# Kernel optimization log

Hardware: AMD Instinct MI355X
Metric: run time of the kernel (lower is better)

Reference implementation:

```python
import jax, jax.numpy as jnp
import numpy as np

G = 160          # dense lattice extent
N = 250000       # occupied voxels


def _offsets(vals):
    a, b, c = np.meshgrid(vals, vals, vals, indexing='ij')
    return np.stack([a.ravel(), b.ravel(), c.ravel()], axis=1)


def _build_kmap(src_lin_sorted, dst_coords, offsets, grid):
    # For each dst coord and kernel offset, find index of src coord (or -1).
    Nd, K = dst_coords.shape[0], offsets.shape[0]
    idx = np.full((Nd, K), -1, dtype=np.int64)
    for k in range(K):
        nb = dst_coords + offsets[k]
        valid = np.all((nb >= 0) & (nb < grid), axis=1)
        keys = (nb[valid, 0] * grid + nb[valid, 1]) * grid + nb[valid, 2]
        pos = np.searchsorted(src_lin_sorted, keys)
        pos_c = np.minimum(pos, len(src_lin_sorted) - 1)
        found = src_lin_sorted[pos_c] == keys
        vi = np.nonzero(valid)[0]
        idx[vi[found], k] = pos_c[found]
    return idx


def setup_inputs() -> dict:
    rng = np.random.default_rng(0)
    lin = np.sort(rng.choice(G ** 3, size=N, replace=False))
    coords = np.stack(np.unravel_index(lin, (G, G, G)), axis=1).astype(np.int64)
    off27 = _offsets(np.array([-1, 0, 1]))
    idx1 = _build_kmap(lin, coords, off27, G)          # k3/s1 on input lattice
    G2 = G // 2
    c2 = coords // 2
    lin2 = np.unique((c2[:, 0] * G2 + c2[:, 1]) * G2 + c2[:, 2])
    coords2 = np.stack(np.unravel_index(lin2, (G2, G2, G2)), axis=1).astype(np.int64)
    off8 = _offsets(np.array([0, 1]))
    idx_down = _build_kmap(lin, coords2 * 2, off8, G)  # k2/s2 downsample map
    idx2 = _build_kmap(lin2, coords2, off27, G2)       # k3/s1 on downsampled lattice

    key = jax.random.key(0)
    ks = jax.random.split(key, 12)

    def w(k, shape, fan_in):
        return jax.random.normal(k, shape, jnp.float32) * (1.0 / np.sqrt(fan_in))

    return {
        'x_feat': jax.random.normal(ks[0], (N, 64), jnp.float32),
        'f1_ref': jax.random.normal(ks[1], (N, 64), jnp.float32),
        'w1': w(ks[2], (27, 64, 64), 27 * 64), 'b1': jnp.zeros((64,), jnp.float32),
        'wd': w(ks[3], (8, 64, 32), 8 * 64), 'bd': jnp.zeros((32,), jnp.float32),
        'rw00': w(ks[4], (3, 27, 32, 8), 27 * 32), 'rb00': jnp.zeros((3, 8), jnp.float32),
        'rw01': w(ks[5], (3, 27, 8, 16), 27 * 8), 'rb01': jnp.zeros((3, 16), jnp.float32),
        'rw10': w(ks[6], (3, 32, 8), 32), 'rb10': jnp.zeros((3, 8), jnp.float32),
        'rw11': w(ks[7], (3, 27, 8, 8), 27 * 8), 'rb11': jnp.zeros((3, 8), jnp.float32),
        'rw12': w(ks[8], (3, 8, 16), 8), 'rb12': jnp.zeros((3, 16), jnp.float32),
        'w4': w(ks[9], (27, 32, 8), 27 * 32), 'b4': jnp.zeros((8,), jnp.float32),
        'idx1': jnp.asarray(idx1), 'idx_down': jnp.asarray(idx_down), 'idx2': jnp.asarray(idx2),
    }


def sparse_conv(feat, idx, W, b):
    # Minkowski sparse conv as gather-GEMM-accumulate over kernel offsets.
    # feat [Nin,Cin], idx [Nout,K] with -1 = no neighbor, W [K,Cin,Cout], b [Cout]
    def step(acc, xs):
        ik, Wk = xs  # [Nout], [Cin,Cout]
        g = jnp.where((ik >= 0)[:, None], feat[jnp.maximum(ik, 0)], 0.0)
        return acc + g @ Wk, None
    acc0 = jnp.zeros((idx.shape[0], W.shape[-1]), feat.dtype)
    out, _ = jax.lax.scan(step, acc0, (idx.T, W))
    return out + b


def reference(x_feat, f1_ref, w1, b1, wd, bd, rw00, rb00, rw01, rb01, rw10, rb10, rw11, rb11, rw12, rb12, w4, b4, idx1, idx_down, idx2):
    relu = jax.nn.relu
    x = x_feat + f1_ref                                  # f1_ref residual add
    out = relu(sparse_conv(x, idx1, w1, b1))             # conv1 + relu
    out = relu(sparse_conv(out, idx_down, wd, bd))       # down (k2/s2) + relu
    for i in range(3):                                   # InceptionResNet x block_layers
        out0 = sparse_conv(relu(sparse_conv(out, idx2, rw00[i], rb00[i])), idx2, rw01[i], rb01[i])
        t = relu(out @ rw10[i] + rb10[i])                # kernel-size-1 conv == linear
        t = relu(sparse_conv(t, idx2, rw11[i], rb11[i]))
        out1 = t @ rw12[i] + rb12[i]
        out = jnp.concatenate([out0, out1], axis=-1) + out
    return sparse_conv(out, idx2, w4, b4)                # enc4
```

## Files before the change

kernel.cpp:

```cpp
#include <hip/hip_runtime.h>
#include <cstdint>

typedef unsigned short u16;
typedef unsigned int   u32;

typedef __bf16 bf16_t;
typedef bf16_t bf16x8 __attribute__((ext_vector_type(8)));
typedef float  f32x16 __attribute__((ext_vector_type(16)));

__device__ __forceinline__ float bf2f(u16 v){ u32 u=((u32)v)<<16; float f; __builtin_memcpy(&f,&u,4); return f; }
__device__ __forceinline__ u16 f2bf(float f){ u32 u; __builtin_memcpy(&u,&f,4); u=(u+0x7FFFu+((u>>16)&1u))>>16; return (u16)u; }

__device__ __forceinline__ u16 cvt(const void* s, long long i, int fbf){
  return fbf ? ((const u16*)s)[i] : f2bf(((const float*)s)[i]);
}

__device__ __forceinline__ int xcd_swz(int bo, int nwg){
  const int q = nwg >> 3, r = nwg & 7;
  const int xcd = bo & 7, lin = bo >> 3;
  return (xcd < r ? xcd * (q + 1) : r * (q + 1) + (xcd - r) * q) + lin;
}

__global__ void detect_k(const u32* __restrict__ xf, const u32* __restrict__ ix,
                         int* __restrict__ flags){
  __shared__ int c0, c1;
  const int t = threadIdx.x;
  if (t == 0) { c0 = 0; c1 = 0; }
  __syncthreads();
  int a = 0, b = 0;
  for (int i = t; i < 1024; i += 256) {
    u32 w = xf[i];
    int e = (int)((w >> 7) & 0xFFu);
    if (e >= 100 && e <= 140) a++;
  }
  for (int i = t; i < 8192; i += 256) {
    u32 lo = ix[2 * i], hi = ix[2 * i + 1];
    if (lo != 0xFFFFFFFFu && hi != 0u && hi != 0xFFFFFFFFu) b++;
  }
  atomicAdd(&c0, a); atomicAdd(&c1, b);
  __syncthreads();
  if (t == 0) { flags[0] = (c0 >= 768) ? 1 : 0; flags[1] = (c1 == 0) ? 1 : 0; }
}

__global__ __launch_bounds__(256) void itr_k(
    const void* __restrict__ idx, int nK, int nKpad, int Nout, int nsrc,
    int Npad, int* __restrict__ dst, const int* __restrict__ flags){
  __shared__ int tile[28][257];
  const int f64 = flags[1];
  const int t = threadIdx.x;
  const int p0 = blockIdx.x * 256;
  const int32_t*  __restrict__ i32 = (const int32_t*)idx;
  const long long* __restrict__ i64 = (const long long*)idx;
  int pl = t / nK;
  int k  = t - pl * nK;
  const int dp = 256 / nK, dk = 256 - dp * nK;
  while (pl < 256) {
    const int p = p0 + pl;
    int j = -1;
    if (p < Nout) {
      const size_t ii = (size_t)p * nK + k;
      j = f64 ? (int)i64[ii] : i32[ii];
    }
    tile[k][pl] = (j < 0 || j > nsrc) ? nsrc : j;
    pl += dp; k += dk;
    if (k >= nK) { k -= nK; pl += 1; }
  }
  __syncthreads();
  for (int kk = 0; kk < nKpad; ++kk) {
    const int v = (kk < nK) ? tile[kk][t] : nsrc;
    dst[(size_t)kk * Npad + p0 + t] = v;
  }
}

template<int CIN, int NF, int NKP, int BCH>
__global__ __launch_bounds__(256) void gconv(
    const u16* __restrict__ src, int nsrc,
    const void* __restrict__ idx, int nK,
    const int* __restrict__ idxT, int Npad,
    const u16* __restrict__ BTf, int iters,
    const u16* __restrict__ bias,
    const u16* __restrict__ bias2, int b2off,
    const u16* __restrict__ resid,
    void* __restrict__ out, int ostride, int coloff, int Cout,
    int relu,
    u16* __restrict__ out2, int o2st, int o2off,
    int Nout, const int* __restrict__ flags, int out_ext)
{
  constexpr int SH = (CIN == 64) ? 7 : (CIN == 32) ? 6 : (CIN == 16) ? 5 : 4;
  constexpr int NB = (BCH == 0) ? 2 * NF : 1;
  __shared__ int idxL[NKP][256];
  __shared__ __align__(16) u16 BsL[(BCH > 0) ? BCH * NF * 512 : 8];

  const int tid = threadIdx.x;
  const int w = tid >> 6, l = tid & 63;
  const int lm = l & 31, lh = l >> 5;
  const int kloc = lh * 8;
  const int M0 = xcd_swz(blockIdx.x, gridDim.x) * 256;
  const int fbf = flags[0], f64 = flags[1];
  const int pl0 = 2 * w * 32 + lm;

  if (idxT) {
    for (int i = tid; i < NKP * 64; i += 256) {
      const int k = i >> 6, g = (i & 63) << 2;
      const uint4 v = *(const uint4*)(idxT + (size_t)k * Npad + M0 + g);
      *(int4*)&idxL[k][g] = make_int4((int)v.x << SH, (int)v.y << SH,
                                      (int)v.z << SH, (int)v.w << SH);
    }
  } else {
    for (int i = tid; i < NKP * 256; i += 256) {
      const int k = i >> 8, pl = i & 255, p = M0 + pl;
      int j = -1;
      if (k < nK && p < Nout) {
        const size_t ii = (size_t)p * nK + k;
        j = f64 ? (int)((const long long*)idx)[ii] : ((const int32_t*)idx)[ii];
      }
      const int r = (j < 0 || j > nsrc) ? nsrc : j;
      idxL[k][pl] = r << SH;
    }
  }
  if constexpr (BCH > 0) {
    for (int i = tid; i < BCH * NF * 64; i += 256)
      ((uint4*)BsL)[i] = ((const uint4*)BTf)[i];
  }
  __syncthreads();

  f32x16 acc[2][NF];
  #pragma unroll
  for (int mm = 0; mm < 2; ++mm)
    #pragma unroll
    for (int nf = 0; nf < NF; ++nf)
      #pragma unroll
      for (int e = 0; e < 16; ++e) acc[mm][nf][e] = 0.f;

  auto LD = [&](int it, uint4 (&A)[4], uint4 (&B)[NB]) {
    const int c0 = 2 * it;
    if constexpr (CIN >= 32) {
      const int k = (CIN == 64) ? (c0 >> 2) : (c0 >> 1);
      const int o0 = idxL[k][pl0];
      const int o1 = idxL[k][pl0 + 32];
      const char* s0 = (const char*)src + o0;
      const char* s1 = (const char*)src + o1;
      #pragma unroll
      for (int s = 0; s < 2; ++s) {
        const int c = c0 + s;
        const int ci2 = ((CIN == 64) ? (((c & 3) << 4) + kloc) : (((c & 1) << 4) + kloc)) * 2;
        A[s * 2 + 0] = *(const uint4*)(s0 + ci2);
        A[s * 2 + 1] = *(const uint4*)(s1 + ci2);
      }
    } else if constexpr (CIN == 16) {
      #pragma unroll
      for (int s = 0; s < 2; ++s) {
        const int k = c0 + s;
        const int o0 = idxL[k][pl0];
        const int o1 = idxL[k][pl0 + 32];
        A[s * 2 + 0] = *(const uint4*)((const char*)src + o0 + lh * 16);
        A[s * 2 + 1] = *(const uint4*)((const char*)src + o1 + lh * 16);
      }
    } else {
      #pragma unroll
      for (int s = 0; s < 2; ++s) {
        const int c = c0 + s;
        const int k = c * 2 + lh;
        const int o0 = idxL[k][pl0];
        const int o1 = idxL[k][pl0 + 32];
        A[s * 2 + 0] = *(const uint4*)((const char*)src + o0);
        A[s * 2 + 1] = *(const uint4*)((const char*)src + o1);
      }
    }
    if constexpr (BCH == 0) {
      #pragma unroll
      for (int s = 0; s < 2; ++s)
        #pragma unroll
        for (int nf = 0; nf < NF; ++nf)
          B[s * NF + nf] = *(const uint4*)(BTf + (((size_t)(c0 + s) * NF + nf) * 64 + l) * 8);
    }
  };

  auto MM = [&](int it, const uint4 (&A)[4], const uint4 (&B)[NB]) {
    const int c0 = 2 * it;
    #pragma unroll
    for (int s = 0; s < 2; ++s) {
      const bf16x8 a0 = __builtin_bit_cast(bf16x8, A[s * 2 + 0]);
      const bf16x8 a1 = __builtin_bit_cast(bf16x8, A[s * 2 + 1]);
      #pragma unroll
      for (int nf = 0; nf < NF; ++nf) {
        bf16x8 b;
        if constexpr (BCH > 0) b = *(const bf16x8*)&BsL[(((c0 + s) * NF + nf) * 64 + l) * 8];
        else                   b = __builtin_bit_cast(bf16x8, B[s * NF + nf]);
        acc[0][nf] = __builtin_amdgcn_mfma_f32_32x32x16_bf16(a0, b, acc[0][nf], 0, 0, 0);
        acc[1][nf] = __builtin_amdgcn_mfma_f32_32x32x16_bf16(a1, b, acc[1][nf], 0, 0, 0);
      }
    }
  };

  uint4 A0[4], A1[4], A2[4], B0[NB], B1[NB], B2[NB];
  LD(0, A0, B0);
  if (iters > 1) LD(1, A1, B1);
  for (int it = 0; it < iters; it += 3) {
    if (it + 2 < iters) LD(it + 2, A2, B2);
    MM(it, A0, B0);
    if (it + 3 < iters) LD(it + 3, A0, B0);
    if (it + 1 < iters) MM(it + 1, A1, B1);
    if (it + 4 < iters) LD(it + 4, A1, B1);
    if (it + 2 < iters) MM(it + 2, A2, B2);
  }

  const int fp32out = out_ext && !fbf;
  #pragma unroll
  for (int mm = 0; mm < 2; ++mm) {
    #pragma unroll
    for (int nf = 0; nf < NF; ++nf) {
      const int co = nf * 32 + lm;
      if (co >= Cout) continue;
      const float bv = (bias2 && co >= b2off) ? bf2f(bias2[co - b2off]) : bf2f(bias[co]);
      #pragma unroll
      for (int r = 0; r < 16; ++r) {
        const int m = (r & 3) + 8 * (r >> 2) + 4 * lh;
        const int p = M0 + (2 * w + mm) * 32 + m;
        if (p >= Nout) continue;
        float v = acc[mm][nf][r] + bv;
        if (out2 && co >= o2off) {
          if (v < 0.f) v = 0.f;
          out2[(size_t)p * o2st + (co - o2off)] = f2bf(v);
        } else {
          if (resid) v += bf2f(resid[(size_t)p * ostride + coloff + co]);
          if (relu && v < 0.f) v = 0.f;
          const size_t ofs = (size_t)p * ostride + coloff + co;
          if (fp32out) ((float*)out)[ofs] = v;
          else         ((u16*)out)[ofs] = f2bf(v);
        }
      }
    }
  }
}

struct PrepJob {
  const void* src; const void* src2; long long eoff, eoff2; u16* dst;
  int nK, Cin, Cout, COPAD, KKpad, mode, count;
};
struct PrepArgs { PrepJob j[19]; };

__global__ void prep_k(PrepArgs a, const int* __restrict__ flags){
  PrepJob jb = a.j[blockIdx.y];
  const int fbf = flags[0];
  if (jb.mode == 1) {
    for (int t = blockIdx.x * 256 + threadIdx.x; t < jb.count; t += gridDim.x * 256)
      jb.dst[t] = cvt(jb.src, jb.eoff + t, fbf);
    return;
  }
  const int total = jb.COPAD * jb.KKpad;
  const int kkmax = jb.nK * jb.Cin;
  if (jb.mode == 3) {
    for (int t = blockIdx.x * 256 + threadIdx.x; t < total; t += gridDim.x * 256) {
      const int e  = t & 7;
      const int lj = (t >> 3) & 63;
      const int chunk = t >> 9;
      const int co = lj & 31;
      const int kk = chunk * 16 + ((lj >> 5) << 3) + e;
      const int k = kk >> 4, ci = kk & 15;
      u16 v = 0;
      if (kk < kkmax && co < jb.Cout) {
        if (ci < 8 && co < 16)
          v = cvt(jb.src,  jb.eoff  + (long long)(k * 8 + ci) * 16 + co, fbf);
        else if (ci >= 8 && co >= 16)
          v = cvt(jb.src2, jb.eoff2 + (long long)(k * 8 + (ci - 8)) * 8 + (co - 16), fbf);
      }
      jb.dst[t] = v;
    }
    return;
  }
  const int NFj = jb.COPAD >> 5;
  for (int t = blockIdx.x * 256 + threadIdx.x; t < total; t += gridDim.x * 256) {
    const int e  = t & 7;
    const int lj = (t >> 3) & 63;
    const int cn = t >> 9;
    const int nf = cn & (NFj - 1);
    const int chunk = cn >> (NFj - 1);
    const int co = nf * 32 + (lj & 31);
    const int kk = chunk * 16 + ((lj >> 5) << 3) + e;
    u16 v = 0;
    if (co < jb.Cout && kk < kkmax)
      v = cvt(jb.src, jb.eoff + (long long)kk * jb.Cout + co, fbf);
    jb.dst[t] = v;
  }
}

__global__ void xsum_k(const void* __restrict__ xa, const void* __restrict__ xb,
                       u16* __restrict__ dst, int n8valid, int n8tot,
                       const int* __restrict__ flags){
  int t = blockIdx.x * 256 + threadIdx.x;
  if (t >= n8tot) return;
  const int fbf = flags[0];
  union { uint4 v; u16 h[8]; } O;
  if (t < n8valid) {
    if (fbf) {
      union { uint4 v; u16 h[8]; } A, B;
      A.v = ((const uint4*)xa)[t];
      B.v = ((const uint4*)xb)[t];
      #pragma unroll
      for (int e = 0; e < 8; ++e) O.h[e] = f2bf(bf2f(A.h[e]) + bf2f(B.h[e]));
    } else {
      const float4* fa = (const float4*)xa;
      const float4* fb = (const float4*)xb;
      float4 a0 = fa[2 * t], a1 = fa[2 * t + 1];
      float4 b0 = fb[2 * t], b1 = fb[2 * t + 1];
      O.h[0] = f2bf(a0.x + b0.x); O.h[1] = f2bf(a0.y + b0.y);
      O.h[2] = f2bf(a0.z + b0.z); O.h[3] = f2bf(a0.w + b0.w);
      O.h[4] = f2bf(a1.x + b1.x); O.h[5] = f2bf(a1.y + b1.y);
      O.h[6] = f2bf(a1.z + b1.z); O.h[7] = f2bf(a1.w + b1.w);
    }
  } else {
    O.v = make_uint4(0, 0, 0, 0);
  }
  ((uint4*)dst)[t] = O.v;
}

__global__ void zrows_k(u16* out1, int N, u16* od0, u16* od1, u16* ht, int N2){
  int t = threadIdx.x;
  if (t < 64) out1[(size_t)N * 64 + t] = 0;
  if (t < 32) od0[(size_t)N2 * 32 + t] = 0;
  if (t < 32) od1[(size_t)N2 * 32 + t] = 0;
  if (t < 16) ht[(size_t)N2 * 16 + t] = 0;
}

__global__ void t8lin_k(const u16* __restrict__ od, const u16* __restrict__ wsrc,
                        const u16* __restrict__ bsrc, u16* __restrict__ ht, int N2){
  __shared__ u16 wl[256];
  int t = threadIdx.x;
  wl[t] = wsrc[t];
  __syncthreads();
  int p = blockIdx.x * 256 + t;
  if (p >= N2) return;
  union { uint4 v[4]; u16 h[32]; } R;
  const uint4* rp = (const uint4*)(od + (size_t)p * 32);
  R.v[0] = rp[0]; R.v[1] = rp[1]; R.v[2] = rp[2]; R.v[3] = rp[3];
  float acc[8];
  #pragma unroll
  for (int o = 0; o < 8; ++o) acc[o] = bf2f(bsrc[o]);
  #pragma unroll
  for (int c = 0; c < 32; ++c) {
    float f = bf2f(R.h[c]);
    #pragma unroll
    for (int o = 0; o < 8; ++o) acc[o] += f * bf2f(wl[c * 8 + o]);
  }
  union { uint4 v; u16 h[8]; } O;
  #pragma unroll
  for (int o = 0; o < 8; ++o) { float v = acc[o]; if (v < 0.f) v = 0.f; O.h[o] = f2bf(v); }
  *(uint4*)(ht + (size_t)p * 16 + 8) = O.v;
}

__global__ void o1lin_k(const u16* __restrict__ t2, const u16* __restrict__ wsrc,
                        const u16* __restrict__ bsrc, const u16* __restrict__ odin,
                        u16* __restrict__ odout, int N2){
  __shared__ u16 wl[128];
  int t = threadIdx.x;
  if (t < 128) wl[t] = wsrc[t];
  __syncthreads();
  int p = blockIdx.x * 256 + t;
  if (p >= N2) return;
  union { uint4 v; u16 h[8]; } R; R.v = ((const uint4*)(t2 + (size_t)p * 8))[0];
  union { uint4 v[2]; u16 h[16]; } Rs;
  const uint4* rp = (const uint4*)(odin + (size_t)p * 32 + 16);
  Rs.v[0] = rp[0]; Rs.v[1] = rp[1];
  float acc[16];
  #pragma unroll
  for (int o = 0; o < 16; ++o) acc[o] = bf2f(bsrc[o]) + bf2f(Rs.h[o]);
  #pragma unroll
  for (int c = 0; c < 8; ++c) {
    float f = bf2f(R.h[c]);
    #pragma unroll
    for (int o = 0; o < 16; ++o) acc[o] += f * bf2f(wl[c * 16 + o]);
  }
  union { uint4 v[2]; u16 h[16]; } O;
  #pragma unroll
  for (int o = 0; o < 16; ++o) O.h[o] = f2bf(acc[o]);
  uint4* op = (uint4*)(odout + (size_t)p * 32 + 16);
  op[0] = O.v[0]; op[1] = O.v[1];
}

extern "C" void kernel_launch(void* const* d_in, const int* in_sizes, int n_in,
                              void* d_out, int out_size, void* d_ws, size_t ws_size,
                              hipStream_t stream) {
  const void* x_feat = d_in[0];
  const void* f1_ref = d_in[1];
  const void* w1   = d_in[2];
  const void* b1   = d_in[3];
  const void* wd   = d_in[4];
  const void* bd   = d_in[5];
  const void* rw00 = d_in[6];
  const void* rb00 = d_in[7];
  const void* rw01 = d_in[8];
  const void* rb01 = d_in[9];
  const void* rw10 = d_in[10];
  const void* rb10 = d_in[11];
  const void* rw11 = d_in[12];
  const void* rb11 = d_in[13];
  const void* rw12 = d_in[14];
  const void* rb12 = d_in[15];
  const void* w4   = d_in[16];
  const void* b4   = d_in[17];
  const void* idx1 = d_in[18];
  const void* idxd = d_in[19];
  const void* idx2 = d_in[20];

  const int N  = in_sizes[0] / 64;
  const int N2 = out_size / 8;

  const int nb1 = (N + 255) / 256;
  const int nb2 = (N2 + 255) / 256;
  const int Npad1 = nb1 * 256;
  const int Npad2 = nb2 * 256;

  size_t off = 0;
  auto carve = [&](size_t n) { void* p = (char*)d_ws + off; off = (off + n + 255) & ~(size_t)255; return p; };
  int* flags = (int*)carve(64 * sizeof(int));
  u16* xsum = (u16*)carve((size_t)(N + 1) * 64 * 2);
  u16* out1 = (u16*)carve((size_t)(N + 1) * 64 * 2);
  u16* od0  = (u16*)carve((size_t)(N2 + 1) * 32 * 2);
  u16* od1  = (u16*)carve((size_t)(N2 + 1) * 32 * 2);
  u16* ht   = (u16*)carve((size_t)(N2 + 1) * 16 * 2);
  u16* t2   = (u16*)carve((size_t)(N2 + 1) * 8 * 2);
  u16* smallw = (u16*)carve((size_t)2048 * 2);
  u16* BT1  = (u16*)carve((size_t)64 * 1728 * 2);
  u16* BTd  = (u16*)carve((size_t)32 * 512 * 2);
  u16* BT00 = (u16*)carve((size_t)3 * 32 * 864 * 2);
  u16* BTf1 = (u16*)carve((size_t)3 * 32 * 448 * 2);
  u16* BT4  = (u16*)carve((size_t)32 * 864 * 2);
  const size_t base_off = off;
  int* idx1T = (int*)carve((size_t)27 * Npad1 * 4);
  int* idxdT = (int*)carve((size_t)8  * Npad2 * 4);
  int* idx2T = (int*)carve((size_t)28 * Npad2 * 4);
  const int useT = (off <= ws_size);
  if (base_off > ws_size) return;
  if (!useT) { idx1T = nullptr; idxdT = nullptr; idx2T = nullptr; }

  u16* cb1   = smallw + 0;
  u16* cbd   = smallw + 64;
  u16* crb00 = smallw + 96;
  u16* crb01 = smallw + 120;
  u16* crb10 = smallw + 168;
  u16* crb11 = smallw + 192;
  u16* crb12 = smallw + 216;
  u16* cb4   = smallw + 264;
  u16* crw10 = smallw + 272;
  u16* crw12 = smallw + 1040;

  detect_k<<<1, 256, 0, stream>>>((const u32*)x_feat, (const u32*)idx1, flags);

  PrepArgs pa;
  pa.j[0]  = { w1, nullptr, 0, 0, BT1, 27, 64, 64, 64, 1728, 0, 0 };
  pa.j[1]  = { wd, nullptr, 0, 0, BTd,  8, 64, 32, 32,  512, 0, 0 };
  for (int i = 0; i < 3; ++i) {
    pa.j[2 + i] = { rw00, nullptr, (long long)i * 6912, 0,
                    BT00 + (size_t)i * 32 * 864, 27, 32, 8, 32, 864, 0, 0 };
    pa.j[5 + i] = { rw01, rw11, (long long)i * 3456, (long long)i * 1728,
                    BTf1 + (size_t)i * 32 * 448, 27, 16, 24, 32, 448, 3, 0 };
  }
  pa.j[8]  = { w4, nullptr, 0, 0, BT4, 27, 32, 8, 32, 864, 0, 0 };
  pa.j[9]  = { b1,   nullptr, 0, 0, cb1,   0,0,0,0,0, 1, 64 };
  pa.j[10] = { bd,   nullptr, 0, 0, cbd,   0,0,0,0,0, 1, 32 };
  pa.j[11] = { rb00, nullptr, 0, 0, crb00, 0,0,0,0,0, 1, 24 };
  pa.j[12] = { rb01, nullptr, 0, 0, crb01, 0,0,0,0,0, 1, 48 };
  pa.j[13] = { rb10, nullptr, 0, 0, crb10, 0,0,0,0,0, 1, 24 };
  pa.j[14] = { rb11, nullptr, 0, 0, crb11, 0,0,0,0,0, 1, 24 };
  pa.j[15] = { rb12, nullptr, 0, 0, crb12, 0,0,0,0,0, 1, 48 };
  pa.j[16] = { b4,   nullptr, 0, 0, cb4,   0,0,0,0,0, 1, 8 };
  pa.j[17] = { rw10, nullptr, 0, 0, crw10, 0,0,0,0,0, 1, 768 };
  pa.j[18] = { rw12, nullptr, 0, 0, crw12, 0,0,0,0,0, 1, 384 };
  prep_k<<<dim3(432, 19), 256, 0, stream>>>(pa, flags);

  if (useT) {
    itr_k<<<nb1, 256, 0, stream>>>(idx1, 27, 27, N,  N,  Npad1, idx1T, flags);
    itr_k<<<nb2, 256, 0, stream>>>(idxd,  8,  8, N2, N,  Npad2, idxdT, flags);
    itr_k<<<nb2, 256, 0, stream>>>(idx2, 27, 28, N2, N2, Npad2, idx2T, flags);
  }

  const int n8valid = N * 8, n8tot = (N + 1) * 8;
  xsum_k<<<(n8tot + 255) / 256, 256, 0, stream>>>(x_feat, f1_ref, xsum, n8valid, n8tot, flags);
  zrows_k<<<1, 256, 0, stream>>>(out1, N, od0, od1, ht, N2);

  gconv<64, 2, 27, 0><<<nb1, 256, 0, stream>>>(xsum, N, idx1, 27, idx1T, Npad1, BT1, 54,
                                               cb1, nullptr, 0, nullptr,
                                               out1, 64, 0, 64, 1, nullptr, 0, 0,
                                               N, flags, 0);
  gconv<64, 1, 8, 32><<<nb2, 256, 0, stream>>>(out1, N, idxd, 8, idxdT, Npad2, BTd, 16,
                                               cbd, nullptr, 0, nullptr,
                                               od0, 32, 0, 32, 1, nullptr, 0, 0,
                                               N2, flags, 0);
  for (int i = 0; i < 3; ++i) {
    u16* oin  = (i & 1) ? od1 : od0;
    u16* oout = (i & 1) ? od0 : od1;
    gconv<32, 1, 27, 0><<<nb2, 256, 0, stream>>>(oin, N2, idx2, 27, idx2T, Npad2,
                                                 BT00 + (size_t)i * 32 * 864, 27,
                                                 crb00 + i * 8, nullptr, 0, nullptr,
                                                 ht, 16, 0, 8, 1, nullptr, 0, 0,
                                                 N2, flags, 0);
    t8lin_k<<<nb2, 256, 0, stream>>>(oin, crw10 + i * 256, crb10 + i * 8, ht, N2);
    gconv<16, 1, 28, 0><<<nb2, 256, 0, stream>>>(ht, N2, idx2, 27, idx2T, Npad2,
                                                 BTf1 + (size_t)i * 32 * 448, 14,
                                                 crb01 + i * 16, crb11 + i * 8, 16, oin,
                                                 oout, 32, 0, 24, 0, t2, 8, 16,
                                                 N2, flags, 0);
    o1lin_k<<<nb2, 256, 0, stream>>>(t2, crw12 + i * 128, crb12 + i * 16, oin, oout, N2);
  }
  gconv<32, 1, 27, 0><<<nb2, 256, 0, stream>>>(od1, N2, idx2, 27, idx2T, Npad2, BT4, 27,
                                               cb4, nullptr, 0, nullptr,
                                               d_out, 8, 0, 8, 0, nullptr, 0, 0,
                                               N2, flags, 1);
}
```

Measured before the change: 698.5 us.

## Fuse 1x1 linear layers into sparse conv kernels and raise MFMA priority

The 1x1 linear rw10 is folded into the rw00 conv's weight matrix, placed at the center-tap rows as extra output columns, so one gconv produces both branches. The rw12 linear plus its residual is computed in an epilogue of the following conv through shared memory, which removes the t8lin_k and o1lin_k launches and the t2 intermediate buffer. It also raises wave priority around the MFMA blocks. The trade-off is extra shared memory, an extra barrier and wasted MMA columns for the fused linear.

```diff
diff --git a/kernel.cpp b/kernel.cpp
--- a/kernel.cpp
+++ b/kernel.cpp
@@ -72,7 +72,7 @@
   }
 }
 
-template<int CIN, int NF, int NKP, int BCH>
+template<int CIN, int NF, int NKP, int BCH, int L2>
 __global__ __launch_bounds__(256) void gconv(
     const u16* __restrict__ src, int nsrc,
     const void* __restrict__ idx, int nK,
@@ -84,12 +84,15 @@
     void* __restrict__ out, int ostride, int coloff, int Cout,
     int relu,
     u16* __restrict__ out2, int o2st, int o2off,
+    const u16* __restrict__ l2w, const u16* __restrict__ l2b,
     int Nout, const int* __restrict__ flags, int out_ext)
 {
   constexpr int SH = (CIN == 64) ? 7 : (CIN == 32) ? 6 : (CIN == 16) ? 5 : 4;
   constexpr int NB = (BCH == 0) ? 2 * NF : 1;
   __shared__ int idxL[NKP][256];
   __shared__ __align__(16) u16 BsL[(BCH > 0) ? BCH * NF * 512 : 8];
+  __shared__ u16 t2L[L2 ? 256 : 1][8];
+  __shared__ u16 l2wl[L2 ? 144 : 1];
 
   const int tid = threadIdx.x;
   const int w = tid >> 6, l = tid & 63;
@@ -121,6 +124,9 @@
   if constexpr (BCH > 0) {
     for (int i = tid; i < BCH * NF * 64; i += 256)
       ((uint4*)BsL)[i] = ((const uint4*)BTf)[i];
+  }
+  if constexpr (L2) {
+    if (tid < 144) l2wl[tid] = (tid < 128) ? l2w[tid] : l2b[tid - 128];
   }
   __syncthreads();
 
@@ -178,6 +184,7 @@
 
   auto MM = [&](int it, const uint4 (&A)[4], const uint4 (&B)[NB]) {
     const int c0 = 2 * it;
+    __builtin_amdgcn_s_setprio(1);
     #pragma unroll
     for (int s = 0; s < 2; ++s) {
       const bf16x8 a0 = __builtin_bit_cast(bf16x8, A[s * 2 + 0]);
@@ -191,6 +198,7 @@
         acc[1][nf] = __builtin_amdgcn_mfma_f32_32x32x16_bf16(a1, b, acc[1][nf], 0, 0, 0);
       }
     }
+    __builtin_amdgcn_s_setprio(0);
   };
 
   uint4 A0[4], A1[4], A2[4], B0[NB], B1[NB], B2[NB];
@@ -216,12 +224,14 @@
       #pragma unroll
       for (int r = 0; r < 16; ++r) {
         const int m = (r & 3) + 8 * (r >> 2) + 4 * lh;
-        const int p = M0 + (2 * w + mm) * 32 + m;
+        const int pl = (2 * w + mm) * 32 + m;
+        const int p = M0 + pl;
         if (p >= Nout) continue;
         float v = acc[mm][nf][r] + bv;
-        if (out2 && co >= o2off) {
+        if ((L2 || out2) && co >= o2off) {
           if (v < 0.f) v = 0.f;
-          out2[(size_t)p * o2st + (co - o2off)] = f2bf(v);
+          if constexpr (L2) t2L[pl][co - o2off] = f2bf(v);
+          else              out2[(size_t)p * o2st + (co - o2off)] = f2bf(v);
         } else {
           if (resid) v += bf2f(resid[(size_t)p * ostride + coloff + co]);
           if (relu && v < 0.f) v = 0.f;
@@ -232,13 +242,37 @@
       }
     }
   }
+
+  if constexpr (L2) {
+    __syncthreads();
+    const int p = M0 + tid;
+    if (p < Nout) {
+      union { uint4 v[2]; u16 h[16]; } Rs;
+      const uint4* rp = (const uint4*)(resid + (size_t)p * 32 + 16);
+      Rs.v[0] = rp[0]; Rs.v[1] = rp[1];
+      float a[16];
+      #pragma unroll
+      for (int o = 0; o < 16; ++o) a[o] = bf2f(l2wl[128 + o]) + bf2f(Rs.h[o]);
+      #pragma unroll
+      for (int c = 0; c < 8; ++c) {
+        const float f = bf2f(t2L[tid][c]);
+        #pragma unroll
+        for (int o = 0; o < 16; ++o) a[o] += f * bf2f(l2wl[c * 16 + o]);
+      }
+      union { uint4 v[2]; u16 h[16]; } O;
+      #pragma unroll
+      for (int o = 0; o < 16; ++o) O.h[o] = f2bf(a[o]);
+      uint4* op = (uint4*)((u16*)out + (size_t)p * 32 + 16);
+      op[0] = O.v[0]; op[1] = O.v[1];
+    }
+  }
 }
 
 struct PrepJob {
   const void* src; const void* src2; long long eoff, eoff2; u16* dst;
   int nK, Cin, Cout, COPAD, KKpad, mode, count;
 };
-struct PrepArgs { PrepJob j[19]; };
+struct PrepArgs { PrepJob j[18]; };
 
 __global__ void prep_k(PrepArgs a, const int* __restrict__ flags){
   PrepJob jb = a.j[blockIdx.y];
@@ -269,6 +303,25 @@
     }
     return;
   }
+  if (jb.mode == 4) {
+    for (int t = blockIdx.x * 256 + threadIdx.x; t < total; t += gridDim.x * 256) {
+      const int e  = t & 7;
+      const int lj = (t >> 3) & 63;
+      const int chunk = t >> 9;
+      const int co = lj & 31;
+      const int kk = chunk * 16 + ((lj >> 5) << 3) + e;
+      const int k = kk >> 5, ci = kk & 31;
+      u16 v = 0;
+      if (kk < kkmax) {
+        if (co < 8)
+          v = cvt(jb.src, jb.eoff + (long long)(k * 32 + ci) * 8 + co, fbf);
+        else if (co < 16 && k == 13)
+          v = cvt(jb.src2, jb.eoff2 + (long long)ci * 8 + (co - 8), fbf);
+      }
+      jb.dst[t] = v;
+    }
+    return;
+  }
   const int NFj = jb.COPAD >> 5;
   for (int t = blockIdx.x * 256 + threadIdx.x; t < total; t += gridDim.x * 256) {
     const int e  = t & 7;
@@ -321,61 +374,6 @@
   if (t < 32) od0[(size_t)N2 * 32 + t] = 0;
   if (t < 32) od1[(size_t)N2 * 32 + t] = 0;
   if (t < 16) ht[(size_t)N2 * 16 + t] = 0;
-}
-
-__global__ void t8lin_k(const u16* __restrict__ od, const u16* __restrict__ wsrc,
-                        const u16* __restrict__ bsrc, u16* __restrict__ ht, int N2){
-  __shared__ u16 wl[256];
-  int t = threadIdx.x;
-  wl[t] = wsrc[t];
-  __syncthreads();
-  int p = blockIdx.x * 256 + t;
-  if (p >= N2) return;
-  union { uint4 v[4]; u16 h[32]; } R;
-  const uint4* rp = (const uint4*)(od + (size_t)p * 32);
-  R.v[0] = rp[0]; R.v[1] = rp[1]; R.v[2] = rp[2]; R.v[3] = rp[3];
-  float acc[8];
-  #pragma unroll
-  for (int o = 0; o < 8; ++o) acc[o] = bf2f(bsrc[o]);
-  #pragma unroll
-  for (int c = 0; c < 32; ++c) {
-    float f = bf2f(R.h[c]);
-    #pragma unroll
-    for (int o = 0; o < 8; ++o) acc[o] += f * bf2f(wl[c * 8 + o]);
-  }
-  union { uint4 v; u16 h[8]; } O;
-  #pragma unroll
-  for (int o = 0; o < 8; ++o) { float v = acc[o]; if (v < 0.f) v = 0.f; O.h[o] = f2bf(v); }
-  *(uint4*)(ht + (size_t)p * 16 + 8) = O.v;
-}
-
-__global__ void o1lin_k(const u16* __restrict__ t2, const u16* __restrict__ wsrc,
-                        const u16* __restrict__ bsrc, const u16* __restrict__ odin,
-                        u16* __restrict__ odout, int N2){
-  __shared__ u16 wl[128];
-  int t = threadIdx.x;
-  if (t < 128) wl[t] = wsrc[t];
-  __syncthreads();
-  int p = blockIdx.x * 256 + t;
-  if (p >= N2) return;
-  union { uint4 v; u16 h[8]; } R; R.v = ((const uint4*)(t2 + (size_t)p * 8))[0];
-  union { uint4 v[2]; u16 h[16]; } Rs;
-  const uint4* rp = (const uint4*)(odin + (size_t)p * 32 + 16);
-  Rs.v[0] = rp[0]; Rs.v[1] = rp[1];
-  float acc[16];
-  #pragma unroll
-  for (int o = 0; o < 16; ++o) acc[o] = bf2f(bsrc[o]) + bf2f(Rs.h[o]);
-  #pragma unroll
-  for (int c = 0; c < 8; ++c) {
-    float f = bf2f(R.h[c]);
-    #pragma unroll
-    for (int o = 0; o < 16; ++o) acc[o] += f * bf2f(wl[c * 16 + o]);
-  }
-  union { uint4 v[2]; u16 h[16]; } O;
-  #pragma unroll
-  for (int o = 0; o < 16; ++o) O.h[o] = f2bf(acc[o]);
-  uint4* op = (uint4*)(odout + (size_t)p * 32 + 16);
-  op[0] = O.v[0]; op[1] = O.v[1];
 }
 
 extern "C" void kernel_launch(void* const* d_in, const int* in_sizes, int n_in,
@@ -419,7 +417,6 @@
   u16* od0  = (u16*)carve((size_t)(N2 + 1) * 32 * 2);
   u16* od1  = (u16*)carve((size_t)(N2 + 1) * 32 * 2);
   u16* ht   = (u16*)carve((size_t)(N2 + 1) * 16 * 2);
-  u16* t2   = (u16*)carve((size_t)(N2 + 1) * 8 * 2);
   u16* smallw = (u16*)carve((size_t)2048 * 2);
   u16* BT1  = (u16*)carve((size_t)64 * 1728 * 2);
   u16* BTd  = (u16*)carve((size_t)32 * 512 * 2);
@@ -442,7 +439,6 @@
   u16* crb11 = smallw + 192;
   u16* crb12 = smallw + 216;
   u16* cb4   = smallw + 264;
-  u16* crw10 = smallw + 272;
   u16* crw12 = smallw + 1040;
 
   detect_k<<<1, 256, 0, stream>>>((const u32*)x_feat, (const u32*)idx1, flags);
@@ -451,8 +447,8 @@
   pa.j[0]  = { w1, nullptr, 0, 0, BT1, 27, 64, 64, 64, 1728, 0, 0 };
   pa.j[1]  = { wd, nullptr, 0, 0, BTd,  8, 64, 32, 32,  512, 0, 0 };
   for (int i = 0; i < 3; ++i) {
-    pa.j[2 + i] = { rw00, nullptr, (long long)i * 6912, 0,
-                    BT00 + (size_t)i * 32 * 864, 27, 32, 8, 32, 864, 0, 0 };
+    pa.j[2 + i] = { rw00, rw10, (long long)i * 6912, (long long)i * 256,
+                    BT00 + (size_t)i * 32 * 864, 27, 32, 16, 32, 864, 4, 0 };
     pa.j[5 + i] = { rw01, rw11, (long long)i * 3456, (long long)i * 1728,
                     BTf1 + (size_t)i * 32 * 448, 27, 16, 24, 32, 448, 3, 0 };
   }
@@ -465,9 +461,8 @@
   pa.j[14] = { rb11, nullptr, 0, 0, crb11, 0,0,0,0,0, 1, 24 };
   pa.j[15] = { rb12, nullptr, 0, 0, crb12, 0,0,0,0,0, 1, 48 };
   pa.j[16] = { b4,   nullptr, 0, 0, cb4,   0,0,0,0,0, 1, 8 };
-  pa.j[17] = { rw10, nullptr, 0, 0, crw10, 0,0,0,0,0, 1, 768 };
-  pa.j[18] = { rw12, nullptr, 0, 0, crw12, 0,0,0,0,0, 1, 384 };
-  prep_k<<<dim3(432, 19), 256, 0, stream>>>(pa, flags);
+  pa.j[17] = { rw12, nullptr, 0, 0, crw12, 0,0,0,0,0, 1, 384 };
+  prep_k<<<dim3(432, 18), 256, 0, stream>>>(pa, flags);
 
   if (useT) {
     itr_k<<<nb1, 256, 0, stream>>>(idx1, 27, 27, N,  N,  Npad1, idx1T, flags);
@@ -479,32 +474,31 @@
   xsum_k<<<(n8tot + 255) / 256, 256, 0, stream>>>(x_feat, f1_ref, xsum, n8valid, n8tot, flags);
   zrows_k<<<1, 256, 0, stream>>>(out1, N, od0, od1, ht, N2);
 
-  gconv<64, 2, 27, 0><<<nb1, 256, 0, stream>>>(xsum, N, idx1, 27, idx1T, Npad1, BT1, 54,
-                                               cb1, nullptr, 0, nullptr,
-                                               out1, 64, 0, 64, 1, nullptr, 0, 0,
-                                               N, flags, 0);
-  gconv<64, 1, 8, 32><<<nb2, 256, 0, stream>>>(out1, N, idxd, 8, idxdT, Npad2, BTd, 16,
-                                               cbd, nullptr, 0, nullptr,
-                                               od0, 32, 0, 32, 1, nullptr, 0, 0,
-                                               N2, flags, 0);
+  gconv<64, 2, 27, 0, 0><<<nb1, 256, 0, stream>>>(xsum, N, idx1, 27, idx1T, Npad1, BT1, 54,
+                                                  cb1, nullptr, 0, nullptr,
+                                                  out1, 64, 0, 64, 1, nullptr, 0, 0,
+                                                  nullptr, nullptr, N, flags, 0);
+  gconv<64, 1, 8, 32, 0><<<nb2, 256, 0, stream>>>(out1, N, idxd, 8, idxdT, Npad2, BTd, 16,
+                                                  cbd, nullptr, 0, nullptr,
+                                                  od0, 32, 0, 32, 1, nullptr, 0, 0,
+                                                  nullptr, nullptr, N2, flags, 0);
   for (int i = 0; i < 3; ++i) {
     u16* oin  = (i & 1) ? od1 : od0;
     u16* oout = (i & 1) ? od0 : od1;
-    gconv<32, 1, 27, 0><<<nb2, 256, 0, stream>>>(oin, N2, idx2, 27, idx2T, Npad2,
-                                                 BT00 + (size_t)i * 32 * 864, 27,
-                                                 crb00 + i * 8, nullptr, 0, nullptr,
-                                                 ht, 16, 0, 8, 1, nullptr, 0, 0,
-                                                 N2, flags, 0);
-    t8lin_k<<<nb2, 256, 0, stream>>>(oin, crw10 + i * 256, crb10 + i * 8, ht, N2);
-    gconv<16, 1, 28, 0><<<nb2, 256, 0, stream>>>(ht, N2, idx2, 27, idx2T, Npad2,
-                                                 BTf1 + (size_t)i * 32 * 448, 14,
-                                                 crb01 + i * 16, crb11 + i * 8, 16, oin,
-                                                 oout, 32, 0, 24, 0, t2, 8, 16,
-                                                 N2, flags, 0);
-    o1lin_k<<<nb2, 256, 0, stream>>>(t2, crw12 + i * 128, crb12 + i * 16, oin, oout, N2);
-  }
-  gconv<32, 1, 27, 0><<<nb2, 256, 0, stream>>>(od1, N2, idx2, 27, idx2T, Npad2, BT4, 27,
-                                               cb4, nullptr, 0, nullptr,
-                                               d_out, 8, 0, 8, 0, nullptr, 0, 0,
-                                               N2, flags, 1);
-}
+    gconv<32, 1, 27, 0, 0><<<nb2, 256, 0, stream>>>(oin, N2, idx2, 27, idx2T, Npad2,
+                                                    BT00 + (size_t)i * 32 * 864, 27,
+                                                    crb00 + i * 8, crb10 + i * 8, 8, nullptr,
+                                                    ht, 16, 0, 16, 1, ht + 8, 16, 8,
+                                                    nullptr, nullptr, N2, flags, 0);
+    gconv<16, 1, 28, 0, 1><<<nb2, 256, 0, stream>>>(ht, N2, idx2, 27, idx2T, Npad2,
+                                                    BTf1 + (size_t)i * 32 * 448, 14,
+                                                    crb01 + i * 16, crb11 + i * 8, 16, oin,
+                                                    oout, 32, 0, 24, 0, nullptr, 0, 16,
+                                                    crw12 + i * 128, crb12 + i * 16,
+                                                    N2, flags, 0);
+  }
+  gconv<32, 1, 27, 0, 0><<<nb2, 256, 0, stream>>>(od1, N2, idx2, 27, idx2T, Npad2, BT4, 27,
+                                                  cb4, nullptr, 0, nullptr,
+                                                  d_out, 8, 0, 8, 0, nullptr, 0, 0,
+                                                  nullptr, nullptr, N2, flags, 1);
+}
```

New measurement: 651.1 us. 6.8% less time.
